# Optimization experiments

Measured on AMD Instinct MI355X. Metric: run time of the kernel, lower is better.

Reference implementation:

```python
import jax, jax.numpy as jnp
import numpy as np

E, D_IN, D_HID, D_OUT, B = 8, 128, 256, 128, 65536


def setup_inputs() -> dict:
    key = jax.random.key(0)
    ks = jax.random.split(key, 6)
    s1 = 1.0 / np.sqrt(D_IN)
    s2 = 1.0 / np.sqrt(D_HID)
    return {
        "x": jax.random.normal(ks[0], (B, D_IN), dtype=jnp.float32),
        "weights": jax.random.uniform(ks[1], (B, E), dtype=jnp.float32),
        "W1": jax.random.uniform(ks[2], (E, D_IN, D_HID), jnp.float32, -s1, s1),
        "b1": jax.random.uniform(ks[3], (E, D_HID), jnp.float32, -s1, s1),
        "W2": jax.random.uniform(ks[4], (E, D_HID, D_OUT), jnp.float32, -s2, s2),
        "b2": jax.random.uniform(ks[5], (E, D_OUT), jnp.float32, -s2, s2),
    }


def reference(x, weights, W1, b1, W2, b2):
    # all-experts dense MLP: every expert processes the full batch
    h = jax.nn.relu(jnp.einsum("bi,eih->beh", x, W1) + b1[None])  # [B,E,H]
    y = jnp.einsum("beh,eho->beo", h, W2) + b2[None]              # [B,E,O]
    # weighted combine over experts
    return jnp.einsum("beo,be->bo", y, weights)                   # [B,O]
```

## Files before the change

kernel.cpp:

```cpp
#include <hip/hip_runtime.h>


#define E_    8
#define DIN_  128
#define DH_   256
#define DOUT_ 128
#define BM_   128
#define NCHUNK 32
#define RECSZ 34816

typedef __attribute__((ext_vector_type(8))) short bf16x8;
typedef __attribute__((ext_vector_type(16))) float f32x16;
typedef __attribute__((ext_vector_type(2))) unsigned int uint2v;

__device__ __forceinline__ unsigned short f2bf(float f) {
  union { float f; unsigned int u; } v; v.f = f;
  unsigned int u = v.u;
  u += 0x7fffu + ((u >> 16) & 1u);
  return (unsigned short)(u >> 16);
}

__device__ __forceinline__ unsigned int cvt_pk_bf16(float lo, float hi) {
  unsigned int r;
  asm("v_cvt_pk_bf16_f32 %0, %1, %2" : "=v"(r) : "v"(lo), "v"(hi));
  return r;
}

__device__ __forceinline__ bf16x8 pack4(unsigned int a, unsigned int b,
                                        unsigned int c, unsigned int d) {
  union { unsigned int u[4]; bf16x8 v; } t;
  t.u[0] = a; t.u[1] = b; t.u[2] = c; t.u[3] = d;
  return t.v;
}

__device__ __forceinline__ void gload_lds16(const void* g, void* l) {
  __builtin_amdgcn_global_load_lds(
      (const __attribute__((address_space(1))) unsigned int*)g,
      (__attribute__((address_space(3))) unsigned int*)l, 16, 0, 0);
}

__global__ __launch_bounds__(256) void prep_pack(
    const float* __restrict__ W1, const float* __restrict__ W2,
    const float* __restrict__ b1, unsigned char* __restrict__ Wall)
{
  __shared__ float T[8192];
  const int bid = blockIdx.x;
  const int t = bid >> 1, region = bid & 1;
  const int e = t >> 2, hc = t & 3;
  const int tid = threadIdx.x;
  unsigned char* rec = Wall + (size_t)t * RECSZ;

  if (region == 0) {
    #pragma unroll
    for (int i = 0; i < 32; ++i) {
      int idx = i * 256 + tid;
      int k = idx >> 6, c = idx & 63;
      T[idx] = W1[((size_t)(e * DIN_ + k)) * DH_ + hc * 64 + c];
    }
    __syncthreads();
    #pragma unroll
    for (int j = 0; j < 16; ++j) {
      int widx = j * 256 + tid;
      int c = widx >> 6, uw = (widx & 63) * 4;
      int up = uw ^ ((c & 7) << 4);
      int k0 = up >> 1;
      unsigned int val = (unsigned int)f2bf(T[k0 * 64 + c]) |
                         ((unsigned int)f2bf(T[(k0 + 1) * 64 + c]) << 16);
      *(unsigned int*)(rec + c * 256 + uw) = val;
    }
    if (tid < 64) {
      *(unsigned int*)(rec + 32768 + tid * 32) =
          (unsigned int)f2bf(b1[e * DH_ + hc * 64 + tid]);
      #pragma unroll
      for (int p = 1; p < 8; ++p)
        *(unsigned int*)(rec + 32768 + tid * 32 + p * 4) = 0u;
    }
  } else {
    #pragma unroll
    for (int i = 0; i < 32; ++i) {
      int idx = i * 256 + tid;
      int h = idx >> 7, n = idx & 127;
      T[idx] = W2[((size_t)(e * DH_ + hc * 64 + h)) * DOUT_ + n];
    }
    __syncthreads();
    #pragma unroll
    for (int j = 0; j < 16; ++j) {
      int widx = j * 256 + tid;
      int n = widx >> 5, uw = (widx & 31) * 4;
      int up = uw ^ ((n & 7) << 4);
      int h0 = up >> 1;
      unsigned int val = (unsigned int)f2bf(T[h0 * 128 + n]) |
                         ((unsigned int)f2bf(T[(h0 + 1) * 128 + n]) << 16);
      *(unsigned int*)(rec + 16384 + n * 128 + uw) = val;
    }
  }
}

__global__ __launch_bounds__(128, 1) void moe_main(
    const float* __restrict__ x, const float* __restrict__ wts,
    const float* __restrict__ b2, const unsigned char* __restrict__ Wall,
    float* __restrict__ out)
{
  __shared__ __align__(16) unsigned char L[2][RECSZ];

  const int tid  = threadIdx.x;
  const int lane = tid & 63;
  const int wv   = tid >> 6;
  const int l32  = lane & 31;
  const int hi   = lane >> 5;
  const int swz  = (l32 & 7) << 4;
  const long bm  = (long)blockIdx.x * BM_;
  const long row0 = bm + wv * 64 + l32;

  auto stage = [&](int t, unsigned char* dst) {
    const unsigned char* src = Wall + (size_t)t * RECSZ;
    #pragma unroll
    for (int r = 0; r < 17; ++r)
      gload_lds16(src + (r * 128 + tid) * 16, dst + r * 2048 + wv * 1024);
  };

  stage(0, L[0]);

  int p1o[8], p2o[4];
  #pragma unroll
  for (int ks = 0; ks < 8; ++ks)
    p1o[ks] = l32 * 256 + ((ks * 32 + hi * 16) ^ swz);
  #pragma unroll
  for (int k2 = 0; k2 < 4; ++k2)
    p2o[k2] = 16384 + l32 * 128 + ((k2 * 32 + hi * 16) ^ swz);
  const int bo = 32768 + l32 * 32 + hi * 16;

  const bf16x8 ones = pack4(hi ? 0u : 0x3F80u, 0u, 0u, 0u);

  bf16x8 xf[2][8];
  #pragma unroll
  for (int mt = 0; mt < 2; ++mt) {
    const float* xr0 = x + (row0 + mt * 32) * DIN_;
    #pragma unroll
    for (int ks = 0; ks < 8; ++ks) {
      const float* xr = xr0 + ks * 16 + hi * 8;
      float4 a = *(const float4*)xr;
      float4 b = *(const float4*)(xr + 4);
      xf[mt][ks] = pack4(cvt_pk_bf16(a.x, a.y), cvt_pk_bf16(a.z, a.w),
                         cvt_pk_bf16(b.x, b.y), cvt_pk_bf16(b.z, b.w));
    }
  }

  const float* wp0 = wts + row0 * E_;
  const float* wp1 = wts + (row0 + 32) * E_;

  f32x16 oacc[2][4];
  #pragma unroll
  for (int mt = 0; mt < 2; ++mt)
    #pragma unroll
    for (int nf = 0; nf < 4; ++nf) oacc[mt][nf] = 0.0f;

  auto chunk = [&](const unsigned char* Lb, int t) {
    const int e = t >> 2;
    const float wA = wp0[e], wB = wp1[e];

    f32x16 h[2][2];
    h[0][0] = 0.0f; h[0][1] = 0.0f; h[1][0] = 0.0f; h[1][1] = 0.0f;
    #pragma unroll
    for (int ks = 0; ks < 8; ++ks) {
      bf16x8 a0 = *(const bf16x8*)(Lb + p1o[ks]);
      bf16x8 a1 = *(const bf16x8*)(Lb + p1o[ks] + 8192);
      h[0][0] = __builtin_amdgcn_mfma_f32_32x32x16_bf16(a0, xf[0][ks], h[0][0], 0, 0, 0);
      h[0][1] = __builtin_amdgcn_mfma_f32_32x32x16_bf16(a0, xf[1][ks], h[0][1], 0, 0, 0);
      h[1][0] = __builtin_amdgcn_mfma_f32_32x32x16_bf16(a1, xf[0][ks], h[1][0], 0, 0, 0);
      h[1][1] = __builtin_amdgcn_mfma_f32_32x32x16_bf16(a1, xf[1][ks], h[1][1], 0, 0, 0);
    }
    {
      bf16x8 bf0 = *(const bf16x8*)(Lb + bo);
      bf16x8 bf1 = *(const bf16x8*)(Lb + bo + 1024);
      h[0][0] = __builtin_amdgcn_mfma_f32_32x32x16_bf16(bf0, ones, h[0][0], 0, 0, 0);
      h[0][1] = __builtin_amdgcn_mfma_f32_32x32x16_bf16(bf0, ones, h[0][1], 0, 0, 0);
      h[1][0] = __builtin_amdgcn_mfma_f32_32x32x16_bf16(bf1, ones, h[1][0], 0, 0, 0);
      h[1][1] = __builtin_amdgcn_mfma_f32_32x32x16_bf16(bf1, ones, h[1][1], 0, 0, 0);
    }

    bf16x8 hfr[2][4];
    #pragma unroll
    for (int mt = 0; mt < 2; ++mt) {
      const float w = mt ? wB : wA;
      #pragma unroll
      for (int cf = 0; cf < 2; ++cf) {
        unsigned int u[8];
        #pragma unroll
        for (int p = 0; p < 8; ++p) {
          float h0 = fmaxf(h[cf][mt][2 * p],     0.0f) * w;
          float h1 = fmaxf(h[cf][mt][2 * p + 1], 0.0f) * w;
          u[p] = cvt_pk_bf16(h0, h1);
        }
        uint2v s02 = __builtin_amdgcn_permlane32_swap(u[0], u[2], false, false);
        uint2v s13 = __builtin_amdgcn_permlane32_swap(u[1], u[3], false, false);
        uint2v s46 = __builtin_amdgcn_permlane32_swap(u[4], u[6], false, false);
        uint2v s57 = __builtin_amdgcn_permlane32_swap(u[5], u[7], false, false);
        hfr[mt][2 * cf]     = pack4(s02[0], s13[0], s02[1], s13[1]);
        hfr[mt][2 * cf + 1] = pack4(s46[0], s57[0], s46[1], s57[1]);
      }
    }

    #pragma unroll
    for (int k2 = 0; k2 < 4; ++k2) {
      #pragma unroll
      for (int nf = 0; nf < 4; ++nf) {
        bf16x8 b = *(const bf16x8*)(Lb + p2o[k2] + nf * 4096);
        oacc[0][nf] = __builtin_amdgcn_mfma_f32_32x32x16_bf16(hfr[0][k2], b, oacc[0][nf], 0, 0, 0);
        oacc[1][nf] = __builtin_amdgcn_mfma_f32_32x32x16_bf16(hfr[1][k2], b, oacc[1][nf], 0, 0, 0);
      }
    }
  };

  for (int tt = 0; tt < NCHUNK; tt += 2) {
    __syncthreads();
    if (tt + 1 < NCHUNK) stage(tt + 1, L[1]);
    chunk(L[0], tt);
    __syncthreads();
    if (tt + 2 < NCHUNK) stage(tt + 2, L[0]);
    chunk(L[1], tt + 1);
  }

  const unsigned int z = 0;
  float wv0[8], wv1[8];
  {
    float4 a = *(const float4*)wp0; float4 b = *(const float4*)(wp0 + 4);
    wv0[0]=a.x; wv0[1]=a.y; wv0[2]=a.z; wv0[3]=a.w;
    wv0[4]=b.x; wv0[5]=b.y; wv0[6]=b.z; wv0[7]=b.w;
    float4 c = *(const float4*)wp1; float4 d = *(const float4*)(wp1 + 4);
    wv1[0]=c.x; wv1[1]=c.y; wv1[2]=c.z; wv1[3]=c.w;
    wv1[4]=d.x; wv1[5]=d.y; wv1[6]=d.z; wv1[7]=d.w;
  }
  bf16x8 wfrag[2];
  wfrag[0] = pack4(hi ? z : cvt_pk_bf16(wv0[0], wv0[1]),
                   hi ? z : cvt_pk_bf16(wv0[2], wv0[3]),
                   hi ? z : cvt_pk_bf16(wv0[4], wv0[5]),
                   hi ? z : cvt_pk_bf16(wv0[6], wv0[7]));
  wfrag[1] = pack4(hi ? z : cvt_pk_bf16(wv1[0], wv1[1]),
                   hi ? z : cvt_pk_bf16(wv1[2], wv1[3]),
                   hi ? z : cvt_pk_bf16(wv1[4], wv1[5]),
                   hi ? z : cvt_pk_bf16(wv1[6], wv1[7]));
  #pragma unroll
  for (int nf = 0; nf < 4; ++nf) {
    const float* bp = b2 + nf * 32 + l32;
    bf16x8 bfrag = pack4(
        hi ? z : cvt_pk_bf16(bp[0 * DOUT_], bp[1 * DOUT_]),
        hi ? z : cvt_pk_bf16(bp[2 * DOUT_], bp[3 * DOUT_]),
        hi ? z : cvt_pk_bf16(bp[4 * DOUT_], bp[5 * DOUT_]),
        hi ? z : cvt_pk_bf16(bp[6 * DOUT_], bp[7 * DOUT_]));
    oacc[0][nf] = __builtin_amdgcn_mfma_f32_32x32x16_bf16(wfrag[0], bfrag, oacc[0][nf], 0, 0, 0);
    oacc[1][nf] = __builtin_amdgcn_mfma_f32_32x32x16_bf16(wfrag[1], bfrag, oacc[1][nf], 0, 0, 0);
  }

  #pragma unroll
  for (int mt = 0; mt < 2; ++mt) {
    #pragma unroll
    for (int nf = 0; nf < 4; ++nf) {
      #pragma unroll
      for (int r = 0; r < 16; ++r) {
        const int mloc = (r & 3) + 8 * (r >> 2) + 4 * hi;
        out[(bm + wv * 64 + mt * 32 + mloc) * DOUT_ + nf * 32 + l32] =
            oacc[mt][nf][r];
      }
    }
  }
}

extern "C" void kernel_launch(void* const* d_in, const int* in_sizes, int n_in,
                              void* d_out, int out_size, void* d_ws, size_t ws_size,
                              hipStream_t stream) {
  const float* x   = (const float*)d_in[0];
  const float* wts = (const float*)d_in[1];
  const float* W1  = (const float*)d_in[2];
  const float* b1  = (const float*)d_in[3];
  const float* W2  = (const float*)d_in[4];
  const float* b2  = (const float*)d_in[5];
  float* out = (float*)d_out;

  unsigned char* Wall = (unsigned char*)d_ws;

  prep_pack<<<64, 256, 0, stream>>>(W1, W2, b1, Wall);
  moe_main<<<65536 / BM_, 128, 0, stream>>>(x, wts, b2, Wall, out);
}
```

Baseline: 95.21 us.

## Split hidden dimension across waves, load W2 fragments directly from global, halve block rows

Row tile drops from 128 to 64, so each block now has two waves that each own half of every 64-wide hidden chunk over the same rows, rather than two waves each owning 64 rows. W2 is pre-packed into a per-lane fragment layout and read straight from global/L2 into registers, so only W1 and b1 go through LDS. This halves LDS per block and permits two blocks per CU. The two waves' partial outputs are summed through LDS at the end, and s_setprio hints are placed around the MFMA sections. The trade is doubled weight traffic per output row and a final cross-wave reduction, in exchange for more occupancy and less LDS read pressure.

```diff
diff --git a/kernel.cpp b/kernel.cpp
--- a/kernel.cpp
+++ b/kernel.cpp
@@ -5,9 +5,9 @@
 #define DIN_  128
 #define DH_   256
 #define DOUT_ 128
-#define BM_   128
+#define BM_   64
 #define NCHUNK 32
-#define RECSZ 34816
+#define REC1  18432
 
 typedef __attribute__((ext_vector_type(8))) short bf16x8;
 typedef __attribute__((ext_vector_type(16))) float f32x16;
@@ -39,69 +39,70 @@
       (__attribute__((address_space(3))) unsigned int*)l, 16, 0, 0);
 }
 
-__global__ __launch_bounds__(256) void prep_pack(
-    const float* __restrict__ W1, const float* __restrict__ W2,
-    const float* __restrict__ b1, unsigned char* __restrict__ Wall)
+__global__ __launch_bounds__(256) void prep_w1(
+    const float* __restrict__ W1, const float* __restrict__ b1,
+    unsigned char* __restrict__ W1r)
 {
   __shared__ float T[8192];
-  const int bid = blockIdx.x;
-  const int t = bid >> 1, region = bid & 1;
+  const int t = blockIdx.x;
   const int e = t >> 2, hc = t & 3;
   const int tid = threadIdx.x;
-  unsigned char* rec = Wall + (size_t)t * RECSZ;
-
-  if (region == 0) {
-    #pragma unroll
-    for (int i = 0; i < 32; ++i) {
-      int idx = i * 256 + tid;
-      int k = idx >> 6, c = idx & 63;
-      T[idx] = W1[((size_t)(e * DIN_ + k)) * DH_ + hc * 64 + c];
-    }
-    __syncthreads();
-    #pragma unroll
-    for (int j = 0; j < 16; ++j) {
-      int widx = j * 256 + tid;
-      int c = widx >> 6, uw = (widx & 63) * 4;
-      int up = uw ^ ((c & 7) << 4);
-      int k0 = up >> 1;
-      unsigned int val = (unsigned int)f2bf(T[k0 * 64 + c]) |
-                         ((unsigned int)f2bf(T[(k0 + 1) * 64 + c]) << 16);
-      *(unsigned int*)(rec + c * 256 + uw) = val;
-    }
-    if (tid < 64) {
-      *(unsigned int*)(rec + 32768 + tid * 32) =
-          (unsigned int)f2bf(b1[e * DH_ + hc * 64 + tid]);
-      #pragma unroll
-      for (int p = 1; p < 8; ++p)
-        *(unsigned int*)(rec + 32768 + tid * 32 + p * 4) = 0u;
-    }
-  } else {
-    #pragma unroll
-    for (int i = 0; i < 32; ++i) {
-      int idx = i * 256 + tid;
-      int h = idx >> 7, n = idx & 127;
-      T[idx] = W2[((size_t)(e * DH_ + hc * 64 + h)) * DOUT_ + n];
-    }
-    __syncthreads();
-    #pragma unroll
-    for (int j = 0; j < 16; ++j) {
-      int widx = j * 256 + tid;
-      int n = widx >> 5, uw = (widx & 31) * 4;
-      int up = uw ^ ((n & 7) << 4);
-      int h0 = up >> 1;
-      unsigned int val = (unsigned int)f2bf(T[h0 * 128 + n]) |
-                         ((unsigned int)f2bf(T[(h0 + 1) * 128 + n]) << 16);
-      *(unsigned int*)(rec + 16384 + n * 128 + uw) = val;
-    }
-  }
-}
-
-__global__ __launch_bounds__(128, 1) void moe_main(
+  unsigned char* rec = W1r + (size_t)t * REC1;
+
+  #pragma unroll
+  for (int i = 0; i < 32; ++i) {
+    int idx = i * 256 + tid;
+    int k = idx >> 6, c = idx & 63;
+    T[idx] = W1[((size_t)(e * DIN_ + k)) * DH_ + hc * 64 + c];
+  }
+  __syncthreads();
+  #pragma unroll
+  for (int j = 0; j < 16; ++j) {
+    int widx = j * 256 + tid;
+    int c = widx >> 6, uw = (widx & 63) * 4;
+    int up = uw ^ ((c & 7) << 4);
+    int k0 = up >> 1;
+    unsigned int val = (unsigned int)f2bf(T[k0 * 64 + c]) |
+                       ((unsigned int)f2bf(T[(k0 + 1) * 64 + c]) << 16);
+    *(unsigned int*)(rec + c * 256 + uw) = val;
+  }
+  if (tid < 64) {
+    *(unsigned int*)(rec + 16384 + tid * 32) =
+        (unsigned int)f2bf(b1[e * DH_ + hc * 64 + tid]);
+    #pragma unroll
+    for (int p = 1; p < 8; ++p)
+      *(unsigned int*)(rec + 16384 + tid * 32 + p * 4) = 0u;
+  }
+}
+
+__global__ __launch_bounds__(256) void prep_w2p(
+    const float* __restrict__ W2, unsigned int* __restrict__ W2p)
+{
+  const int t = blockIdx.x;
+  const int e = t >> 2, hc = t & 3;
+  const int tid = threadIdx.x;
+  unsigned int* outw = W2p + (size_t)t * 4096;
+  #pragma unroll
+  for (int j = 0; j < 16; ++j) {
+    int w = j * 256 + tid;
+    int wh = w >> 11, k2 = (w >> 10) & 1, nf = (w >> 8) & 3;
+    int lane = (w >> 2) & 63, pr = w & 3;
+    int hi = lane >> 5, l32 = lane & 31;
+    int n = nf * 32 + l32;
+    int c = hc * 64 + wh * 32 + k2 * 16 + hi * 8 + pr * 2;
+    unsigned int val =
+        (unsigned int)f2bf(W2[((size_t)(e * DH_ + c)) * DOUT_ + n]) |
+        ((unsigned int)f2bf(W2[((size_t)(e * DH_ + c + 1)) * DOUT_ + n]) << 16);
+    outw[w] = val;
+  }
+}
+
+__global__ __launch_bounds__(128, 2) void moe_main(
     const float* __restrict__ x, const float* __restrict__ wts,
-    const float* __restrict__ b2, const unsigned char* __restrict__ Wall,
-    float* __restrict__ out)
+    const float* __restrict__ b2, const unsigned char* __restrict__ W1r,
+    const unsigned char* __restrict__ W2p, float* __restrict__ out)
 {
-  __shared__ __align__(16) unsigned char L[2][RECSZ];
+  __shared__ __align__(16) unsigned char L[2][REC1];
 
   const int tid  = threadIdx.x;
   const int lane = tid & 63;
@@ -110,32 +111,28 @@
   const int hi   = lane >> 5;
   const int swz  = (l32 & 7) << 4;
   const long bm  = (long)blockIdx.x * BM_;
-  const long row0 = bm + wv * 64 + l32;
 
   auto stage = [&](int t, unsigned char* dst) {
-    const unsigned char* src = Wall + (size_t)t * RECSZ;
-    #pragma unroll
-    for (int r = 0; r < 17; ++r)
+    const unsigned char* src = W1r + (size_t)t * REC1;
+    #pragma unroll
+    for (int r = 0; r < 9; ++r)
       gload_lds16(src + (r * 128 + tid) * 16, dst + r * 2048 + wv * 1024);
   };
 
   stage(0, L[0]);
 
-  int p1o[8], p2o[4];
+  int p1o[8];
   #pragma unroll
   for (int ks = 0; ks < 8; ++ks)
-    p1o[ks] = l32 * 256 + ((ks * 32 + hi * 16) ^ swz);
-  #pragma unroll
-  for (int k2 = 0; k2 < 4; ++k2)
-    p2o[k2] = 16384 + l32 * 128 + ((k2 * 32 + hi * 16) ^ swz);
-  const int bo = 32768 + l32 * 32 + hi * 16;
+    p1o[ks] = (wv * 32 + l32) * 256 + ((ks * 32 + hi * 16) ^ swz);
+  const int bo = 16384 + (wv * 32 + l32) * 32 + hi * 16;
 
   const bf16x8 ones = pack4(hi ? 0u : 0x3F80u, 0u, 0u, 0u);
 
   bf16x8 xf[2][8];
   #pragma unroll
   for (int mt = 0; mt < 2; ++mt) {
-    const float* xr0 = x + (row0 + mt * 32) * DIN_;
+    const float* xr0 = x + (bm + mt * 32 + l32) * DIN_;
     #pragma unroll
     for (int ks = 0; ks < 8; ++ks) {
       const float* xr = xr0 + ks * 16 + hi * 8;
@@ -146,8 +143,8 @@
     }
   }
 
-  const float* wp0 = wts + row0 * E_;
-  const float* wp1 = wts + (row0 + 32) * E_;
+  const float* wp0 = wts + (bm + l32) * E_;
+  const float* wp1 = wts + (bm + 32 + l32) * E_;
 
   f32x16 oacc[2][4];
   #pragma unroll
@@ -155,114 +152,134 @@
     #pragma unroll
     for (int nf = 0; nf < 4; ++nf) oacc[mt][nf] = 0.0f;
 
-  auto chunk = [&](const unsigned char* Lb, int t) {
+  for (int t = 0; t < NCHUNK; ++t) {
     const int e = t >> 2;
+    __syncthreads();
+    if (t + 1 < NCHUNK) stage(t + 1, L[(t + 1) & 1]);
+    const unsigned char* Lb = L[t & 1];
+
+    bf16x8 w2f[8];
+    {
+      const unsigned char* wb = W2p + (size_t)t * 16384 + wv * 8192 + lane * 16;
+      #pragma unroll
+      for (int i = 0; i < 8; ++i)
+        w2f[i] = *(const bf16x8*)(wb + i * 1024);
+    }
     const float wA = wp0[e], wB = wp1[e];
-
-    f32x16 h[2][2];
-    h[0][0] = 0.0f; h[0][1] = 0.0f; h[1][0] = 0.0f; h[1][1] = 0.0f;
+    bf16x8 bfr = *(const bf16x8*)(Lb + bo);
+
+    f32x16 h0 = 0.0f, h1 = 0.0f;
+    __builtin_amdgcn_s_setprio(1);
     #pragma unroll
     for (int ks = 0; ks < 8; ++ks) {
-      bf16x8 a0 = *(const bf16x8*)(Lb + p1o[ks]);
-      bf16x8 a1 = *(const bf16x8*)(Lb + p1o[ks] + 8192);
-      h[0][0] = __builtin_amdgcn_mfma_f32_32x32x16_bf16(a0, xf[0][ks], h[0][0], 0, 0, 0);
-      h[0][1] = __builtin_amdgcn_mfma_f32_32x32x16_bf16(a0, xf[1][ks], h[0][1], 0, 0, 0);
-      h[1][0] = __builtin_amdgcn_mfma_f32_32x32x16_bf16(a1, xf[0][ks], h[1][0], 0, 0, 0);
-      h[1][1] = __builtin_amdgcn_mfma_f32_32x32x16_bf16(a1, xf[1][ks], h[1][1], 0, 0, 0);
-    }
+      bf16x8 a = *(const bf16x8*)(Lb + p1o[ks]);
+      h0 = __builtin_amdgcn_mfma_f32_32x32x16_bf16(a, xf[0][ks], h0, 0, 0, 0);
+      h1 = __builtin_amdgcn_mfma_f32_32x32x16_bf16(a, xf[1][ks], h1, 0, 0, 0);
+    }
+    h0 = __builtin_amdgcn_mfma_f32_32x32x16_bf16(bfr, ones, h0, 0, 0, 0);
+    h1 = __builtin_amdgcn_mfma_f32_32x32x16_bf16(bfr, ones, h1, 0, 0, 0);
+    __builtin_amdgcn_s_setprio(0);
+
+    bf16x8 hfr0[2], hfr1[2];
+    #pragma unroll
+    for (int mt = 0; mt < 2; ++mt) {
+      const f32x16& hh = mt ? h1 : h0;
+      const float w = mt ? wB : wA;
+      unsigned int u[8];
+      #pragma unroll
+      for (int p = 0; p < 8; ++p) {
+        float a = fmaxf(hh[2 * p],     0.0f) * w;
+        float b = fmaxf(hh[2 * p + 1], 0.0f) * w;
+        u[p] = cvt_pk_bf16(a, b);
+      }
+      uint2v s02 = __builtin_amdgcn_permlane32_swap(u[0], u[2], false, false);
+      uint2v s13 = __builtin_amdgcn_permlane32_swap(u[1], u[3], false, false);
+      uint2v s46 = __builtin_amdgcn_permlane32_swap(u[4], u[6], false, false);
+      uint2v s57 = __builtin_amdgcn_permlane32_swap(u[5], u[7], false, false);
+      bf16x8 f0 = pack4(s02[0], s13[0], s02[1], s13[1]);
+      bf16x8 f1 = pack4(s46[0], s57[0], s46[1], s57[1]);
+      if (mt) { hfr1[0] = f0; hfr1[1] = f1; }
+      else    { hfr0[0] = f0; hfr0[1] = f1; }
+    }
+
+    __builtin_amdgcn_s_setprio(1);
+    #pragma unroll
+    for (int k2 = 0; k2 < 2; ++k2) {
+      #pragma unroll
+      for (int nf = 0; nf < 4; ++nf) {
+        bf16x8 b = w2f[k2 * 4 + nf];
+        oacc[0][nf] = __builtin_amdgcn_mfma_f32_32x32x16_bf16(hfr0[k2], b, oacc[0][nf], 0, 0, 0);
+        oacc[1][nf] = __builtin_amdgcn_mfma_f32_32x32x16_bf16(hfr1[k2], b, oacc[1][nf], 0, 0, 0);
+      }
+    }
+    __builtin_amdgcn_s_setprio(0);
+  }
+
+  __syncthreads();
+  float* X = (float*)&L[0][0];
+  if (wv == 1) {
+    #pragma unroll
+    for (int mt = 0; mt < 2; ++mt)
+      #pragma unroll
+      for (int nf = 0; nf < 4; ++nf)
+        #pragma unroll
+        for (int r = 0; r < 16; ++r) {
+          const int mloc = (r & 3) + 8 * (r >> 2) + 4 * hi;
+          X[(mt * 32 + mloc) * DOUT_ + nf * 32 + l32] = oacc[mt][nf][r];
+        }
+  }
+  __syncthreads();
+  if (wv == 0) {
+    #pragma unroll
+    for (int mt = 0; mt < 2; ++mt)
+      #pragma unroll
+      for (int nf = 0; nf < 4; ++nf)
+        #pragma unroll
+        for (int r = 0; r < 16; ++r) {
+          const int mloc = (r & 3) + 8 * (r >> 2) + 4 * hi;
+          oacc[mt][nf][r] += X[(mt * 32 + mloc) * DOUT_ + nf * 32 + l32];
+        }
+
+    const unsigned int z = 0;
+    float wv0[8], wv1[8];
     {
-      bf16x8 bf0 = *(const bf16x8*)(Lb + bo);
-      bf16x8 bf1 = *(const bf16x8*)(Lb + bo + 1024);
-      h[0][0] = __builtin_amdgcn_mfma_f32_32x32x16_bf16(bf0, ones, h[0][0], 0, 0, 0);
-      h[0][1] = __builtin_amdgcn_mfma_f32_32x32x16_bf16(bf0, ones, h[0][1], 0, 0, 0);
-      h[1][0] = __builtin_amdgcn_mfma_f32_32x32x16_bf16(bf1, ones, h[1][0], 0, 0, 0);
-      h[1][1] = __builtin_amdgcn_mfma_f32_32x32x16_bf16(bf1, ones, h[1][1], 0, 0, 0);
-    }
-
-    bf16x8 hfr[2][4];
-    #pragma unroll
-    for (int mt = 0; mt < 2; ++mt) {
-      const float w = mt ? wB : wA;
-      #pragma unroll
-      for (int cf = 0; cf < 2; ++cf) {
-        unsigned int u[8];
+      float4 a = *(const float4*)wp0; float4 b = *(const float4*)(wp0 + 4);
+      wv0[0]=a.x; wv0[1]=a.y; wv0[2]=a.z; wv0[3]=a.w;
+      wv0[4]=b.x; wv0[5]=b.y; wv0[6]=b.z; wv0[7]=b.w;
+      float4 c = *(const float4*)wp1; float4 d = *(const float4*)(wp1 + 4);
+      wv1[0]=c.x; wv1[1]=c.y; wv1[2]=c.z; wv1[3]=c.w;
+      wv1[4]=d.x; wv1[5]=d.y; wv1[6]=d.z; wv1[7]=d.w;
+    }
+    bf16x8 wfrag[2];
+    wfrag[0] = pack4(hi ? z : cvt_pk_bf16(wv0[0], wv0[1]),
+                     hi ? z : cvt_pk_bf16(wv0[2], wv0[3]),
+                     hi ? z : cvt_pk_bf16(wv0[4], wv0[5]),
+                     hi ? z : cvt_pk_bf16(wv0[6], wv0[7]));
+    wfrag[1] = pack4(hi ? z : cvt_pk_bf16(wv1[0], wv1[1]),
+                     hi ? z : cvt_pk_bf16(wv1[2], wv1[3]),
+                     hi ? z : cvt_pk_bf16(wv1[4], wv1[5]),
+                     hi ? z : cvt_pk_bf16(wv1[6], wv1[7]));
+    #pragma unroll
+    for (int nf = 0; nf < 4; ++nf) {
+      const float* bp = b2 + nf * 32 + l32;
+      bf16x8 bfrag = pack4(
+          hi ? z : cvt_pk_bf16(bp[0 * DOUT_], bp[1 * DOUT_]),
+          hi ? z : cvt_pk_bf16(bp[2 * DOUT_], bp[3 * DOUT_]),
+          hi ? z : cvt_pk_bf16(bp[4 * DOUT_], bp[5 * DOUT_]),
+          hi ? z : cvt_pk_bf16(bp[6 * DOUT_], bp[7 * DOUT_]));
+      oacc[0][nf] = __builtin_amdgcn_mfma_f32_32x32x16_bf16(wfrag[0], bfrag, oacc[0][nf], 0, 0, 0);
+      oacc[1][nf] = __builtin_amdgcn_mfma_f32_32x32x16_bf16(wfrag[1], bfrag, oacc[1][nf], 0, 0, 0);
+    }
+
+    #pragma unroll
+    for (int mt = 0; mt < 2; ++mt)
+      #pragma unroll
+      for (int nf = 0; nf < 4; ++nf)
         #pragma unroll
-        for (int p = 0; p < 8; ++p) {
-          float h0 = fmaxf(h[cf][mt][2 * p],     0.0f) * w;
-          float h1 = fmaxf(h[cf][mt][2 * p + 1], 0.0f) * w;
-          u[p] = cvt_pk_bf16(h0, h1);
+        for (int r = 0; r < 16; ++r) {
+          const int mloc = (r & 3) + 8 * (r >> 2) + 4 * hi;
+          out[(bm + mt * 32 + mloc) * DOUT_ + nf * 32 + l32] = oacc[mt][nf][r];
         }
-        uint2v s02 = __builtin_amdgcn_permlane32_swap(u[0], u[2], false, false);
-        uint2v s13 = __builtin_amdgcn_permlane32_swap(u[1], u[3], false, false);
-        uint2v s46 = __builtin_amdgcn_permlane32_swap(u[4], u[6], false, false);
-        uint2v s57 = __builtin_amdgcn_permlane32_swap(u[5], u[7], false, false);
-        hfr[mt][2 * cf]     = pack4(s02[0], s13[0], s02[1], s13[1]);
-        hfr[mt][2 * cf + 1] = pack4(s46[0], s57[0], s46[1], s57[1]);
-      }
-    }
-
-    #pragma unroll
-    for (int k2 = 0; k2 < 4; ++k2) {
-      #pragma unroll
-      for (int nf = 0; nf < 4; ++nf) {
-        bf16x8 b = *(const bf16x8*)(Lb + p2o[k2] + nf * 4096);
-        oacc[0][nf] = __builtin_amdgcn_mfma_f32_32x32x16_bf16(hfr[0][k2], b, oacc[0][nf], 0, 0, 0);
-        oacc[1][nf] = __builtin_amdgcn_mfma_f32_32x32x16_bf16(hfr[1][k2], b, oacc[1][nf], 0, 0, 0);
-      }
-    }
-  };
-
-  for (int tt = 0; tt < NCHUNK; tt += 2) {
-    __syncthreads();
-    if (tt + 1 < NCHUNK) stage(tt + 1, L[1]);
-    chunk(L[0], tt);
-    __syncthreads();
-    if (tt + 2 < NCHUNK) stage(tt + 2, L[0]);
-    chunk(L[1], tt + 1);
-  }
-
-  const unsigned int z = 0;
-  float wv0[8], wv1[8];
-  {
-    float4 a = *(const float4*)wp0; float4 b = *(const float4*)(wp0 + 4);
-    wv0[0]=a.x; wv0[1]=a.y; wv0[2]=a.z; wv0[3]=a.w;
-    wv0[4]=b.x; wv0[5]=b.y; wv0[6]=b.z; wv0[7]=b.w;
-    float4 c = *(const float4*)wp1; float4 d = *(const float4*)(wp1 + 4);
-    wv1[0]=c.x; wv1[1]=c.y; wv1[2]=c.z; wv1[3]=c.w;
-    wv1[4]=d.x; wv1[5]=d.y; wv1[6]=d.z; wv1[7]=d.w;
-  }
-  bf16x8 wfrag[2];
-  wfrag[0] = pack4(hi ? z : cvt_pk_bf16(wv0[0], wv0[1]),
-                   hi ? z : cvt_pk_bf16(wv0[2], wv0[3]),
-                   hi ? z : cvt_pk_bf16(wv0[4], wv0[5]),
-                   hi ? z : cvt_pk_bf16(wv0[6], wv0[7]));
-  wfrag[1] = pack4(hi ? z : cvt_pk_bf16(wv1[0], wv1[1]),
-                   hi ? z : cvt_pk_bf16(wv1[2], wv1[3]),
-                   hi ? z : cvt_pk_bf16(wv1[4], wv1[5]),
-                   hi ? z : cvt_pk_bf16(wv1[6], wv1[7]));
-  #pragma unroll
-  for (int nf = 0; nf < 4; ++nf) {
-    const float* bp = b2 + nf * 32 + l32;
-    bf16x8 bfrag = pack4(
-        hi ? z : cvt_pk_bf16(bp[0 * DOUT_], bp[1 * DOUT_]),
-        hi ? z : cvt_pk_bf16(bp[2 * DOUT_], bp[3 * DOUT_]),
-        hi ? z : cvt_pk_bf16(bp[4 * DOUT_], bp[5 * DOUT_]),
-        hi ? z : cvt_pk_bf16(bp[6 * DOUT_], bp[7 * DOUT_]));
-    oacc[0][nf] = __builtin_amdgcn_mfma_f32_32x32x16_bf16(wfrag[0], bfrag, oacc[0][nf], 0, 0, 0);
-    oacc[1][nf] = __builtin_amdgcn_mfma_f32_32x32x16_bf16(wfrag[1], bfrag, oacc[1][nf], 0, 0, 0);
-  }
-
-  #pragma unroll
-  for (int mt = 0; mt < 2; ++mt) {
-    #pragma unroll
-    for (int nf = 0; nf < 4; ++nf) {
-      #pragma unroll
-      for (int r = 0; r < 16; ++r) {
-        const int mloc = (r & 3) + 8 * (r >> 2) + 4 * hi;
-        out[(bm + wv * 64 + mt * 32 + mloc) * DOUT_ + nf * 32 + l32] =
-            oacc[mt][nf][r];
-      }
-    }
   }
 }
 
@@ -277,8 +294,10 @@
   const float* b2  = (const float*)d_in[5];
   float* out = (float*)d_out;
 
-  unsigned char* Wall = (unsigned char*)d_ws;
-
-  prep_pack<<<64, 256, 0, stream>>>(W1, W2, b1, Wall);
-  moe_main<<<65536 / BM_, 128, 0, stream>>>(x, wts, b2, Wall, out);
-}
+  unsigned char* W1r = (unsigned char*)d_ws;
+  unsigned char* W2p = W1r + (size_t)NCHUNK * REC1;
+
+  prep_w1<<<32, 256, 0, stream>>>(W1, b1, W1r);
+  prep_w2p<<<32, 256, 0, stream>>>(W2, (unsigned int*)W2p);
+  moe_main<<<65536 / BM_, 128, 0, stream>>>(x, wts, b2, W1r, W2p, out);
+}
```

Result: slower. 161.6 us (+69.7%).
